# Performance work log

Hardware: AMD Instinct MI355X
Metric: run time of the kernel (lower is better)

## Reference

```python
import jax, jax.numpy as jnp
import numpy as np

SIM_THRESHOLD = 0.7
EPS = 1e-8  # matches torch F.cosine_similarity eps

Q, M, D, C = 4096, 65536, 384, 128


def setup_inputs() -> dict:
    key = jax.random.key(0)
    k1, k2, k3 = jax.random.split(key, 3)
    query_embeddings = jax.random.normal(k1, (Q, D), dtype=jnp.float32)
    memory_embeddings = jax.random.normal(k2, (M, D), dtype=jnp.float32)
    # per-example one-hot-ish label vectors [M, C]
    memory_labels = jax.random.uniform(k3, (M, C), dtype=jnp.float32)
    return {
        "query_embeddings": query_embeddings,
        "memory_embeddings": memory_embeddings,
        "memory_labels": memory_labels,
    }


def _l2_normalize(x):
    n = jnp.sqrt(jnp.sum(x * x, axis=-1, keepdims=True))
    return x / jnp.maximum(n, EPS)


def reference(query_embeddings, memory_embeddings, memory_labels):
    # cosine similarity matrix [Q, M] via normalized GEMM
    qn = _l2_normalize(query_embeddings)          # [Q, D]
    mn = _l2_normalize(memory_embeddings)         # [M, D]
    sims = jnp.einsum("qd,md->qm", qn, mn)        # [Q, M]
    max_sim = jnp.max(sims, axis=1)               # [Q]
    max_idx = jnp.argmax(sims, axis=1)            # [Q]
    picked = memory_labels[max_idx]               # [Q, C] gather
    C_ = memory_labels.shape[1]
    uniform = jnp.full((1, C_), 1.0 / C_, dtype=picked.dtype)
    predictions = jnp.where((max_sim > SIM_THRESHOLD)[:, None], picked, uniform)
    return predictions
```

## Files before the change

kernel.cpp:

```cpp
#include <hip/hip_runtime.h>
#include <math.h>

#define QN 4096
#define MN 65536
#define DN 384
#define CN 128
#define NCHUNK 64
#define MROWS_PER_CHUNK (MN / NCHUNK)
#define MT_PER (MROWS_PER_CHUNK / 64)
#define FRAG_B 1024
#define GSTRIDE (3 * FRAG_B)
#define TSTRIDE (4 * GSTRIDE)

typedef __attribute__((ext_vector_type(8))) int i32x8;
typedef __attribute__((ext_vector_type(4))) int i32x4;
typedef __attribute__((ext_vector_type(4))) float f32x4;

__device__ __forceinline__ unsigned fp4e(float x) {
  const float a = fabsf(x);
  unsigned c = (unsigned)(a >= 0.25f) + (a >= 0.75f) + (a >= 1.25f) +
               (a >= 1.75f) + (a >= 2.5f) + (a >= 3.5f) + (a >= 5.0f);
  return ((x < 0.f) ? 8u : 0u) | c;
}

__global__ __launch_bounds__(256) void nrm_kernel(const float* __restrict__ qe,
                                                  const float* __restrict__ me,
                                                  unsigned char* __restrict__ yq,
                                                  unsigned char* __restrict__ ym) {
  const int row = blockIdx.x * 4 + (threadIdx.x >> 6);
  const int lane = threadIdx.x & 63;
  const int isq = (row < QN);
  const int r = isq ? row : row - QN;
  const float* xr = isq ? qe + (size_t)r * DN : me + (size_t)r * DN;
  unsigned char* yb = isq ? yq : ym;
  float2 v[3];
  float ss = 0.f;
#pragma unroll
  for (int i = 0; i < 3; ++i) {
    v[i] = *(const float2*)&xr[lane * 2 + i * 128];
    ss += v[i].x * v[i].x + v[i].y * v[i].y;
  }
#pragma unroll
  for (int m = 1; m < 64; m <<= 1) ss += __shfl_xor(ss, m);
  const float s16 = (16.0f / fmaxf(sqrtf(ss), 1e-8f));
  const int g = r >> 4;
  const int fl = ((lane >> 4) << 4) + (r & 15);
#pragma unroll
  for (int i = 0; i < 3; ++i) {
    const unsigned b = fp4e(v[i].x * s16) | (fp4e(v[i].y * s16) << 4);
    yb[((size_t)(g * 3 + i) * 64 + fl) * 16 + (lane & 15)] = (unsigned char)b;
  }
}

__global__ __launch_bounds__(256, 2) void gemm_max_kernel(
    const unsigned char* __restrict__ qn4, const unsigned char* __restrict__ mn4,
    float* __restrict__ pmax) {
  __shared__ float smax[2][128];

  const int tid = threadIdx.x;
  const int wave = tid >> 6, lane = tid & 63;
  const int wr = wave >> 1, wc = wave & 1;
  const int quad = lane >> 4, l16 = lane & 15;

  const int bid = blockIdx.y * gridDim.x + blockIdx.x;
  const int xcd = bid & 7;
  const int j = bid >> 3;
  const int ychunk = (xcd << 3) | (j >> 5);
  const int qrow0 = (j & 31) * 128;
  const int mchunk0 = ychunk * MROWS_PER_CHUNK;

  float rmax[16];
#pragma unroll
  for (int i = 0; i < 16; ++i) rmax[i] = -3.0e38f;

  const int gq0 = (qrow0 >> 4) + wr * 4;
  i32x8 afr[3][4];
#pragma unroll
  for (int kc = 0; kc < 3; ++kc)
#pragma unroll
    for (int rt = 0; rt < 4; ++rt) {
      afr[kc][rt] = (i32x8){0, 0, 0, 0, 0, 0, 0, 0};
      i32x4 t = *(const i32x4*)(qn4 +
          ((size_t)((gq0 + rt) * 3 + kc) * 64 + lane) * 16);
      afr[kc][rt][0] = t[0]; afr[kc][rt][1] = t[1];
      afr[kc][rt][2] = t[2]; afr[kc][rt][3] = t[3];
    }

  const int g0 = (mchunk0 >> 4) + wc * 2;
  const unsigned char* bp0 = mn4 + ((size_t)g0 * 3 * 64 + lane) * 16;
  const unsigned char* bp1 = bp0 + GSTRIDE;

  i32x8 pre[3], b1[3];
#pragma unroll
  for (int kc = 0; kc < 3; ++kc) {
    pre[kc] = (i32x8){0, 0, 0, 0, 0, 0, 0, 0};
    b1[kc] = (i32x8){0, 0, 0, 0, 0, 0, 0, 0};
  }
#pragma unroll
  for (int kc = 0; kc < 3; ++kc) {
    i32x4 t = *(const i32x4*)(bp0 + kc * FRAG_B);
    pre[kc][0] = t[0]; pre[kc][1] = t[1]; pre[kc][2] = t[2]; pre[kc][3] = t[3];
  }
  bp0 += TSTRIDE;

#pragma unroll 1
  for (int mt = 0; mt < MT_PER; ++mt) {
#pragma unroll
    for (int kc = 0; kc < 3; ++kc) {
      i32x4 t = *(const i32x4*)(bp1 + kc * FRAG_B);
      b1[kc][0] = t[0]; b1[kc][1] = t[1]; b1[kc][2] = t[2]; b1[kc][3] = t[3];
    }
    bp1 += TSTRIDE;
    __builtin_amdgcn_sched_barrier(0);

    {
      f32x4 acc[4];
#pragma unroll
      for (int rt = 0; rt < 4; ++rt) acc[rt] = (f32x4){0.f, 0.f, 0.f, 0.f};
      __builtin_amdgcn_s_setprio(1);
#pragma unroll
      for (int kc = 0; kc < 3; ++kc)
#pragma unroll
        for (int rt = 0; rt < 4; ++rt)
          acc[rt] = __builtin_amdgcn_mfma_scale_f32_16x16x128_f8f6f4(
              afr[kc][rt], pre[kc], acc[rt], 4, 4,
              0, 0x7b7b7b7b, 0, 0x7b7b7b7b);
      __builtin_amdgcn_s_setprio(0);
#pragma unroll
      for (int rt = 0; rt < 4; ++rt)
#pragma unroll
        for (int r = 0; r < 4; ++r)
          rmax[rt * 4 + r] = fmaxf(rmax[rt * 4 + r], acc[rt][r]);
    }
    __builtin_amdgcn_sched_barrier(0);

    if (mt + 1 < MT_PER) {
#pragma unroll
      for (int kc = 0; kc < 3; ++kc) {
        i32x4 t = *(const i32x4*)(bp0 + kc * FRAG_B);
        pre[kc][0] = t[0]; pre[kc][1] = t[1];
        pre[kc][2] = t[2]; pre[kc][3] = t[3];
      }
      bp0 += TSTRIDE;
    }
    __builtin_amdgcn_sched_barrier(0);

    {
      f32x4 acc[4];
#pragma unroll
      for (int rt = 0; rt < 4; ++rt) acc[rt] = (f32x4){0.f, 0.f, 0.f, 0.f};
      __builtin_amdgcn_s_setprio(1);
#pragma unroll
      for (int kc = 0; kc < 3; ++kc)
#pragma unroll
        for (int rt = 0; rt < 4; ++rt)
          acc[rt] = __builtin_amdgcn_mfma_scale_f32_16x16x128_f8f6f4(
              afr[kc][rt], b1[kc], acc[rt], 4, 4,
              0, 0x7b7b7b7b, 0, 0x7b7b7b7b);
      __builtin_amdgcn_s_setprio(0);
#pragma unroll
      for (int rt = 0; rt < 4; ++rt)
#pragma unroll
        for (int r = 0; r < 4; ++r)
          rmax[rt * 4 + r] = fmaxf(rmax[rt * 4 + r], acc[rt][r]);
    }
  }

#pragma unroll
  for (int i = 0; i < 16; ++i) {
    float v = rmax[i];
    v = fmaxf(v, __shfl_xor(v, 1));
    v = fmaxf(v, __shfl_xor(v, 2));
    v = fmaxf(v, __shfl_xor(v, 4));
    v = fmaxf(v, __shfl_xor(v, 8));
    rmax[i] = v;
  }
  if (l16 == 0) {
#pragma unroll
    for (int rt = 0; rt < 4; ++rt)
#pragma unroll
      for (int r = 0; r < 4; ++r)
        smax[wc][wr * 64 + rt * 16 + quad * 4 + r] = rmax[rt * 4 + r];
  }
  __syncthreads();
  if (tid < 128) {
    const float v = fmaxf(smax[0][tid], smax[1][tid]);
    pmax[(size_t)(qrow0 + tid) * NCHUNK + ychunk] = v;
  }
}

__global__ __launch_bounds__(256) void decide_kernel(
    const float* __restrict__ pmax, const float* __restrict__ qe,
    const float* __restrict__ me, const float* __restrict__ labels,
    float* __restrict__ out) {
  const int q = blockIdx.x;
  const int t = threadIdx.x;
  __shared__ float smx;
  if (t < 64) {
    float v = pmax[(size_t)q * NCHUNK + t];
#pragma unroll
    for (int m = 1; m < 64; m <<= 1) v = fmaxf(v, __shfl_xor(v, m));
    if (t == 0) smx = v;
  }
  __syncthreads();
  if (smx <= 0.5f) {
    if (t < CN) out[(size_t)q * CN + t] = 1.0f / 128.0f;
    return;
  }
  __shared__ float sred[256];
  __shared__ int sidx[256];
  __shared__ float wsum[4];
  const float* qr = qe + (size_t)q * DN;
  float ss = 0.f;
  for (int i = t; i < DN; i += 256) ss += qr[i] * qr[i];
#pragma unroll
  for (int m = 1; m < 64; m <<= 1) ss += __shfl_xor(ss, m);
  if ((t & 63) == 0) wsum[t >> 6] = ss;
  __syncthreads();
  const float qnorm = fmaxf(sqrtf(wsum[0] + wsum[1] + wsum[2] + wsum[3]), 1e-8f);

  float best = -3.0e38f;
  int bidx = 0x7fffffff;
  for (int j = t; j < MN; j += 256) {
    const float* mr = me + (size_t)j * DN;
    float dot = 0.f, ms = 0.f;
    for (int k = 0; k < DN; ++k) {
      float a = qr[k], b = mr[k];
      dot += a * b;
      ms += b * b;
    }
    const float sim = dot / (qnorm * fmaxf(sqrtf(ms), 1e-8f));
    if (sim > best) { best = sim; bidx = j; }
  }
  sred[t] = best;
  sidx[t] = bidx;
  __syncthreads();
  for (int s = 128; s > 0; s >>= 1) {
    if (t < s) {
      const float ov = sred[t + s];
      const int oi = sidx[t + s];
      if (ov > sred[t] || (ov == sred[t] && oi < sidx[t])) {
        sred[t] = ov;
        sidx[t] = oi;
      }
    }
    __syncthreads();
  }
  const float mx = sred[0];
  const int mi = sidx[0];
  if (t < CN)
    out[(size_t)q * CN + t] =
        (mx > 0.7f) ? labels[(size_t)mi * CN + t] : (1.0f / 128.0f);
}

extern "C" void kernel_launch(void* const* d_in, const int* in_sizes, int n_in,
                              void* d_out, int out_size, void* d_ws,
                              size_t ws_size, hipStream_t stream) {
  const float* qe = (const float*)d_in[0];
  const float* me = (const float*)d_in[1];
  const float* lb = (const float*)d_in[2];
  float* out = (float*)d_out;

  char* ws = (char*)d_ws;
  const size_t OFF_QN = 0;
  const size_t OFF_MN = OFF_QN + (size_t)QN * DN;
  const size_t OFF_PMAX = OFF_MN + (size_t)MN * DN;
  unsigned char* qn4 = (unsigned char*)(ws + OFF_QN);
  unsigned char* mn4 = (unsigned char*)(ws + OFF_MN);
  float* pmax = (float*)(ws + OFF_PMAX);

  nrm_kernel<<<(QN + MN) / 4, 256, 0, stream>>>(qe, me, qn4, mn4);
  gemm_max_kernel<<<dim3(QN / 128, NCHUNK), 256, 0, stream>>>(qn4, mn4, pmax);
  decide_kernel<<<QN, 256, 0, stream>>>(pmax, qe, me, lb, out);
}
```

Baseline: 212.0 us.

## Switch FP4 similarity GEMM to 32x32x64 scaled MFMA with matching fragment layout

Replaces the 16x16x128 scaled FP4 MFMA tiles with 32x32x64 tiles. The normalization kernel's packed layout is rebuilt around 32-row groups with six K-chunks, and the row-max reduction and shared-memory writeback are remapped to the 32x32 output layout. Each 64-wide M step now accumulates across two halves into one accumulator pair, so the max update runs once per iteration instead of twice. The aim is fewer MFMA issues and fewer max/VALU ops per tile, at the cost of larger accumulators (32 rmax registers) and more complex index mapping that could affect occupancy or correctness.

```diff
diff --git a/kernel.cpp b/kernel.cpp
--- a/kernel.cpp
+++ b/kernel.cpp
@@ -9,12 +9,12 @@
 #define MROWS_PER_CHUNK (MN / NCHUNK)
 #define MT_PER (MROWS_PER_CHUNK / 64)
 #define FRAG_B 1024
-#define GSTRIDE (3 * FRAG_B)
-#define TSTRIDE (4 * GSTRIDE)
+#define GSTRIDE6 (6 * FRAG_B)
+#define TSTRIDE32 (2 * GSTRIDE6)
 
 typedef __attribute__((ext_vector_type(8))) int i32x8;
 typedef __attribute__((ext_vector_type(4))) int i32x4;
-typedef __attribute__((ext_vector_type(4))) float f32x4;
+typedef __attribute__((ext_vector_type(16))) float f32x16;
 
 __device__ __forceinline__ unsigned fp4e(float x) {
   const float a = fabsf(x);
@@ -43,12 +43,14 @@
 #pragma unroll
   for (int m = 1; m < 64; m <<= 1) ss += __shfl_xor(ss, m);
   const float s16 = (16.0f / fmaxf(sqrtf(ss), 1e-8f));
-  const int g = r >> 4;
-  const int fl = ((lane >> 4) << 4) + (r & 15);
+  const int g32 = r >> 5;
+  const int fl = ((lane >> 4) & 1) * 32 + (r & 31);
+  const int kcb = lane >> 5;
 #pragma unroll
   for (int i = 0; i < 3; ++i) {
     const unsigned b = fp4e(v[i].x * s16) | (fp4e(v[i].y * s16) << 4);
-    yb[((size_t)(g * 3 + i) * 64 + fl) * 16 + (lane & 15)] = (unsigned char)b;
+    yb[((size_t)(g32 * 6 + kcb + 2 * i) * 64 + fl) * 16 + (lane & 15)] =
+        (unsigned char)b;
   }
 }
 
@@ -60,7 +62,6 @@
   const int tid = threadIdx.x;
   const int wave = tid >> 6, lane = tid & 63;
   const int wr = wave >> 1, wc = wave & 1;
-  const int quad = lane >> 4, l16 = lane & 15;
 
   const int bid = blockIdx.y * gridDim.x + blockIdx.x;
   const int xcd = bid & 7;
@@ -69,26 +70,26 @@
   const int qrow0 = (j & 31) * 128;
   const int mchunk0 = ychunk * MROWS_PER_CHUNK;
 
-  float rmax[16];
-#pragma unroll
-  for (int i = 0; i < 16; ++i) rmax[i] = -3.0e38f;
-
-  const int gq0 = (qrow0 >> 4) + wr * 4;
-  i32x8 afr[3][4];
-#pragma unroll
-  for (int kc = 0; kc < 3; ++kc)
-#pragma unroll
-    for (int rt = 0; rt < 4; ++rt) {
+  float rmax[32];
+#pragma unroll
+  for (int i = 0; i < 32; ++i) rmax[i] = -3.0e38f;
+
+  const int gq0 = (qrow0 >> 5) + wr * 2;
+  i32x8 afr[6][2];
+#pragma unroll
+  for (int kc = 0; kc < 6; ++kc)
+#pragma unroll
+    for (int rt = 0; rt < 2; ++rt) {
       afr[kc][rt] = (i32x8){0, 0, 0, 0, 0, 0, 0, 0};
       i32x4 t = *(const i32x4*)(qn4 +
-          ((size_t)((gq0 + rt) * 3 + kc) * 64 + lane) * 16);
+          ((size_t)((gq0 + rt) * 6 + kc) * 64 + lane) * 16);
       afr[kc][rt][0] = t[0]; afr[kc][rt][1] = t[1];
       afr[kc][rt][2] = t[2]; afr[kc][rt][3] = t[3];
     }
 
-  const int g0 = (mchunk0 >> 4) + wc * 2;
-  const unsigned char* bp0 = mn4 + ((size_t)g0 * 3 * 64 + lane) * 16;
-  const unsigned char* bp1 = bp0 + GSTRIDE;
+  const int gm0 = (mchunk0 >> 5) + wc;
+  const unsigned char* bp = mn4 + ((size_t)gm0 * 6 * 64 + lane) * 16;
+  const unsigned char* bq = bp + 3 * FRAG_B;
 
   i32x8 pre[3], b1[3];
 #pragma unroll
@@ -98,89 +99,85 @@
   }
 #pragma unroll
   for (int kc = 0; kc < 3; ++kc) {
-    i32x4 t = *(const i32x4*)(bp0 + kc * FRAG_B);
+    i32x4 t = *(const i32x4*)(bp + kc * FRAG_B);
     pre[kc][0] = t[0]; pre[kc][1] = t[1]; pre[kc][2] = t[2]; pre[kc][3] = t[3];
   }
-  bp0 += TSTRIDE;
+  bp += TSTRIDE32;
 
 #pragma unroll 1
   for (int mt = 0; mt < MT_PER; ++mt) {
 #pragma unroll
     for (int kc = 0; kc < 3; ++kc) {
-      i32x4 t = *(const i32x4*)(bp1 + kc * FRAG_B);
+      i32x4 t = *(const i32x4*)(bq + kc * FRAG_B);
       b1[kc][0] = t[0]; b1[kc][1] = t[1]; b1[kc][2] = t[2]; b1[kc][3] = t[3];
     }
-    bp1 += TSTRIDE;
+    bq += TSTRIDE32;
     __builtin_amdgcn_sched_barrier(0);
 
-    {
-      f32x4 acc[4];
-#pragma unroll
-      for (int rt = 0; rt < 4; ++rt) acc[rt] = (f32x4){0.f, 0.f, 0.f, 0.f};
-      __builtin_amdgcn_s_setprio(1);
-#pragma unroll
-      for (int kc = 0; kc < 3; ++kc)
-#pragma unroll
-        for (int rt = 0; rt < 4; ++rt)
-          acc[rt] = __builtin_amdgcn_mfma_scale_f32_16x16x128_f8f6f4(
-              afr[kc][rt], pre[kc], acc[rt], 4, 4,
-              0, 0x7b7b7b7b, 0, 0x7b7b7b7b);
-      __builtin_amdgcn_s_setprio(0);
-#pragma unroll
-      for (int rt = 0; rt < 4; ++rt)
-#pragma unroll
-        for (int r = 0; r < 4; ++r)
-          rmax[rt * 4 + r] = fmaxf(rmax[rt * 4 + r], acc[rt][r]);
-    }
+    f32x16 acc0 = (f32x16)(0.f), acc1 = (f32x16)(0.f);
+
+    __builtin_amdgcn_s_setprio(1);
+#pragma unroll
+    for (int kc = 0; kc < 3; ++kc) {
+      acc0 = __builtin_amdgcn_mfma_scale_f32_32x32x64_f8f6f4(
+          afr[kc][0], pre[kc], acc0, 4, 4,
+          0, 0x7b7b7b7b, 0, 0x7b7b7b7b);
+      acc1 = __builtin_amdgcn_mfma_scale_f32_32x32x64_f8f6f4(
+          afr[kc][1], pre[kc], acc1, 4, 4,
+          0, 0x7b7b7b7b, 0, 0x7b7b7b7b);
+    }
+    __builtin_amdgcn_s_setprio(0);
     __builtin_amdgcn_sched_barrier(0);
 
     if (mt + 1 < MT_PER) {
 #pragma unroll
       for (int kc = 0; kc < 3; ++kc) {
-        i32x4 t = *(const i32x4*)(bp0 + kc * FRAG_B);
+        i32x4 t = *(const i32x4*)(bp + kc * FRAG_B);
         pre[kc][0] = t[0]; pre[kc][1] = t[1];
         pre[kc][2] = t[2]; pre[kc][3] = t[3];
       }
-      bp0 += TSTRIDE;
+      bp += TSTRIDE32;
     }
     __builtin_amdgcn_sched_barrier(0);
 
-    {
-      f32x4 acc[4];
-#pragma unroll
-      for (int rt = 0; rt < 4; ++rt) acc[rt] = (f32x4){0.f, 0.f, 0.f, 0.f};
-      __builtin_amdgcn_s_setprio(1);
-#pragma unroll
-      for (int kc = 0; kc < 3; ++kc)
-#pragma unroll
-        for (int rt = 0; rt < 4; ++rt)
-          acc[rt] = __builtin_amdgcn_mfma_scale_f32_16x16x128_f8f6f4(
-              afr[kc][rt], b1[kc], acc[rt], 4, 4,
-              0, 0x7b7b7b7b, 0, 0x7b7b7b7b);
-      __builtin_amdgcn_s_setprio(0);
-#pragma unroll
-      for (int rt = 0; rt < 4; ++rt)
-#pragma unroll
-        for (int r = 0; r < 4; ++r)
-          rmax[rt * 4 + r] = fmaxf(rmax[rt * 4 + r], acc[rt][r]);
-    }
-  }
-
-#pragma unroll
-  for (int i = 0; i < 16; ++i) {
+    __builtin_amdgcn_s_setprio(1);
+#pragma unroll
+    for (int kc = 0; kc < 3; ++kc) {
+      acc0 = __builtin_amdgcn_mfma_scale_f32_32x32x64_f8f6f4(
+          afr[kc + 3][0], b1[kc], acc0, 4, 4,
+          0, 0x7b7b7b7b, 0, 0x7b7b7b7b);
+      acc1 = __builtin_amdgcn_mfma_scale_f32_32x32x64_f8f6f4(
+          afr[kc + 3][1], b1[kc], acc1, 4, 4,
+          0, 0x7b7b7b7b, 0, 0x7b7b7b7b);
+    }
+    __builtin_amdgcn_s_setprio(0);
+
+#pragma unroll
+    for (int r = 0; r < 16; ++r) {
+      rmax[r] = fmaxf(rmax[r], acc0[r]);
+      rmax[16 + r] = fmaxf(rmax[16 + r], acc1[r]);
+    }
+  }
+
+#pragma unroll
+  for (int i = 0; i < 32; ++i) {
     float v = rmax[i];
     v = fmaxf(v, __shfl_xor(v, 1));
     v = fmaxf(v, __shfl_xor(v, 2));
     v = fmaxf(v, __shfl_xor(v, 4));
     v = fmaxf(v, __shfl_xor(v, 8));
+    v = fmaxf(v, __shfl_xor(v, 16));
     rmax[i] = v;
   }
-  if (l16 == 0) {
-#pragma unroll
-    for (int rt = 0; rt < 4; ++rt)
-#pragma unroll
-      for (int r = 0; r < 4; ++r)
-        smax[wc][wr * 64 + rt * 16 + quad * 4 + r] = rmax[rt * 4 + r];
+  if ((lane & 31) == 0) {
+    const int h4 = (lane >> 5) * 4;
+#pragma unroll
+    for (int rt = 0; rt < 2; ++rt)
+#pragma unroll
+      for (int reg = 0; reg < 16; ++reg) {
+        const int qiw = rt * 32 + (reg & 3) + 8 * (reg >> 2) + h4;
+        smax[wc][wr * 64 + qiw] = rmax[rt * 16 + reg];
+      }
   }
   __syncthreads();
   if (tid < 128) {
```

Result: slower. 229.9 us (+8.4%).
